# Optimization experiments

Measured on AMD Instinct MI355X. Metric: run time of the kernel, lower is better.

The kernel has to match this reference:

```python
import jax, jax.numpy as jnp
import numpy as np

B, R, L, D, V, P = 128, 30, 60, 300, 50000, 3

def setup_inputs() -> dict:
    key = jax.random.key(0)
    ks = jax.random.split(key, 24)
    u = lambda k, shp: jax.random.uniform(k, shp, jnp.float32, -0.1, 0.1)
    inp = {
        'user_reviews': jax.random.randint(ks[0], (B, R, L), 0, V),
        'item_reviews': jax.random.randint(ks[1], (B, R, L), 0, V),
        'user_emb': u(ks[2], (V, D)),
        'item_emb': u(ks[3], (V, D)),
        'g1_w': u(ks[4], (D, D)), 'g1_b': u(ks[5], (D,)),
        'g2_w': u(ks[6], (D, D)), 'g2_b': u(ks[7], (D,)),
        # per-pointer review-level co-attention params (gumbel=True, pooling=max)
        'Mr': jax.random.normal(ks[8], (P, D, D)),
        'Wur': jax.random.normal(ks[9], (P, D, D)) * 0.05, 'bur': jnp.zeros((P, D)),
        'Wir': jax.random.normal(ks[10], (P, D, D)) * 0.05, 'bir': jnp.zeros((P, D)),
        # per-pointer word-level co-attention params (gumbel=False, pooling=avg)
        'Mw': jax.random.normal(ks[11], (P, D, D)),
        'Wuw': jax.random.normal(ks[12], (P, D, D)) * 0.05, 'buw': jnp.zeros((P, D)),
        'Wiw': jax.random.normal(ks[13], (P, D, D)) * 0.05, 'biw': jnp.zeros((P, D)),
        # FM params, pred_in_dim = 2*P*D (pointer_agg='concat')
        'fm_w0': jnp.zeros((1,)),
        'fm_w': jnp.zeros((2 * P * D,)),
        'fm_v': jax.random.normal(ks[14], (2 * P * D, 10)) * 0.01,
    }
    return inp

def _review_gate(embs, g1_w, g1_b, g2_w, g2_b):
    # embs: [B,R,L,D] -> [B,R,D]
    s = embs.sum(2)
    return jax.nn.sigmoid(s @ g1_w.T + g1_b) * jnp.tanh(s @ g2_w.T + g2_b)

def _coatt_scores(u_fea, i_fea, Wu, bu, Wi, bi, M):
    u = u_fea @ Wu.T + bu
    i = i_fea @ Wi.T + bi
    return jnp.einsum('brd,de,bse->brs', u, M, i)  # [B,R,R] or [B,L,L]

def reference(user_reviews, item_reviews, user_emb, item_emb,
              g1_w, g1_b, g2_w, g2_b,
              Mr, Wur, bur, Wir, bir,
              Mw, Wuw, buw, Wiw, biw,
              fm_w0, fm_w, fm_v):
    gkey = jax.random.key(42)
    u_embs = user_emb[user_reviews]  # [B,R,L,D]
    i_embs = item_emb[item_reviews]
    u_rev = _review_gate(u_embs, g1_w, g1_b, g2_w, g2_b)  # [B,R,D]
    i_rev = _review_gate(i_embs, g1_w, g1_b, g2_w, g2_b)
    u_reps, i_reps = [], []
    for p in range(P):
        # review-level co-attention, max pooling, gumbel hard (top-1 pointer)
        s = _coatt_scores(u_rev, i_rev, Wur[p], bur[p], Wir[p], bir[p], Mr[p])
        u_score = s.max(2)   # [B,R]
        i_score = s.max(1)   # [B,R]
        gu = jax.random.gumbel(jax.random.fold_in(gkey, 2 * p), u_score.shape)
        gi = jax.random.gumbel(jax.random.fold_in(gkey, 2 * p + 1), i_score.shape)
        # hard one-hot bmm gather + .long() re-embed == argmax review select
        # (the .long() cast in torch severs the straight-through grad path)
        idx_u = jnp.argmax(u_score + gu, axis=1)  # [B]
        idx_i = jnp.argmax(i_score + gi, axis=1)
        u_tok = jnp.take_along_axis(user_reviews, idx_u[:, None, None], axis=1)[:, 0]  # [B,L]
        i_tok = jnp.take_along_axis(item_reviews, idx_i[:, None, None], axis=1)[:, 0]
        u_words = user_emb[u_tok]  # [B,L,D]
        i_words = item_emb[i_tok]
        # word-level co-attention, avg pooling, soft attention
        s2 = _coatt_scores(u_words, i_words, Wuw[p], buw[p], Wiw[p], biw[p], Mw[p])
        p_u = jax.nn.softmax(s2.mean(2), axis=1)  # [B,L]
        p_i = jax.nn.softmax(s2.mean(1), axis=1)
        u_reps.append(jnp.einsum('bld,bl->bd', u_words, p_u))
        i_reps.append(jnp.einsum('bld,bl->bd', i_words, p_i))
    u_fea = jnp.concatenate(u_reps, axis=1)  # [B, P*D] (pointer_agg='concat')
    i_fea = jnp.concatenate(i_reps, axis=1)
    joint = jnp.concatenate([u_fea, i_fea], axis=1)  # [B, 2*P*D]; dropout is identity (eval)
    # Factorization Machine
    linear = fm_w0 + jnp.sum(fm_w * joint, axis=1, keepdims=True)
    inter = 0.5 * jnp.sum((joint @ fm_v) ** 2 - (joint ** 2) @ (fm_v ** 2), axis=1, keepdims=True)
    return (linear + inter)[:, 0]  # [B]
```

## Files before the change

kernel.cpp:

```cpp
#include <hip/hip_runtime.h>
#include <stdint.h>
#include <math.h>


__host__ __device__ static inline void tf2x32(uint32_t k0, uint32_t k1,
                                              uint32_t x0, uint32_t x1,
                                              uint32_t* o0, uint32_t* o1) {
  uint32_t ks[3] = {k0, k1, k0 ^ k1 ^ 0x1BD11BDAu};
  x0 += ks[0]; x1 += ks[1];
  const int rotA[4] = {13, 15, 26, 6};
  const int rotB[4] = {17, 29, 16, 24};
#pragma unroll
  for (int i = 0; i < 5; ++i) {
    const int* rot = ((i & 1) == 0) ? rotA : rotB;
#pragma unroll
    for (int j = 0; j < 4; ++j) {
      x0 += x1;
      x1 = (x1 << rot[j]) | (x1 >> (32 - rot[j]));
      x1 ^= x0;
    }
    x0 += ks[(i + 1) % 3];
    x1 += ks[(i + 2) % 3] + (uint32_t)(i + 1);
  }
  *o0 = x0; *o1 = x1;
}

struct GKeys { uint32_t v[12]; };
struct Ptr6 {
  const float* X[6];
  const float* W[6];
  const float* Bb[6];
  float*       Y[6];
};

__device__ static inline float jax_gumbel32(uint32_t k0, uint32_t k1, uint32_t idx) {
  uint32_t o0, o1;
  tf2x32(k0, k1, 0u, idx, &o0, &o1);
  uint32_t bits = o0 ^ o1;
  float f = __uint_as_float((bits >> 9) | 0x3f800000u) - 1.0f;
  float u = (f > 0.0f) ? f : 1.17549435e-38f;
  return -logf(-logf(u));
}

#define MODE_NN 0
#define MODE_NT 1
#define MODE_TN 2

template <int MODE, bool BIAS>
__device__ __forceinline__ void gemm_tile(float* __restrict__ sm,
                                          const float* __restrict__ X,
                                          const float* __restrict__ W,
                                          const float* __restrict__ bias,
                                          float* __restrict__ Y,
                                          float* __restrict__ Yt,
                                          int M, int bm, int n0, int t) {
  float (*Xs)[68] = (float(*)[68])sm;
  float (*Ws_)[68] = (float(*)[68])(sm + 20 * 68);
  const bool act = t < 256;
  int tm4 = ((t >> 4) & 15) * 4;
  int tn4 = (t & 15) * 4;
  float acc[4][4] = {{0.f}};
  int xm = t >> 2;
  int xk = (t & 3) * 5;
  for (int k0 = 0; k0 < 300; k0 += 20) {
    if (act) {
      if (MODE == MODE_TN) {
#pragma unroll
        for (int i = 0; i < 5; ++i) {
          int flat = t + i * 256;
          int kk = flat >> 6, nn = flat & 63;
          int r = bm + nn;
          Xs[kk][nn] = (r < 300) ? X[(size_t)(k0 + kk) * 300 + r] : 0.f;
        }
      } else {
        int rr = bm + xm; if (rr >= M) rr = M - 1;
        const float* xp = X + (size_t)rr * 300 + k0 + xk;
#pragma unroll
        for (int j = 0; j < 5; ++j) Xs[xk + j][xm] = xp[j];
      }
      if (MODE == MODE_NT) {
        int d = n0 + xm;
        bool ok = d < 300;
        const float* wp = W + (size_t)d * 300 + k0 + xk;
#pragma unroll
        for (int j = 0; j < 5; ++j) Ws_[xk + j][xm] = ok ? wp[j] : 0.f;
      } else {
#pragma unroll
        for (int i = 0; i < 5; ++i) {
          int flat = t + i * 256;
          int kk = flat >> 6, nn = flat & 63;
          int col = n0 + nn;
          Ws_[kk][nn] = (col < 300) ? W[(size_t)(k0 + kk) * 300 + col] : 0.f;
        }
      }
    }
    __syncthreads();
    if (act) {
#pragma unroll
      for (int kk = 0; kk < 20; ++kk) {
        const float4 a = *(const float4*)&Xs[kk][tm4];
        const float4 w = *(const float4*)&Ws_[kk][tn4];
        float av[4] = {a.x, a.y, a.z, a.w};
        float wv[4] = {w.x, w.y, w.z, w.w};
#pragma unroll
        for (int i = 0; i < 4; ++i)
#pragma unroll
          for (int j = 0; j < 4; ++j)
            acc[i][j] = fmaf(av[i], wv[j], acc[i][j]);
      }
    }
    __syncthreads();
  }
  if (!act) return;
  float bv[4] = {0.f, 0.f, 0.f, 0.f};
  if (BIAS) {
#pragma unroll
    for (int j = 0; j < 4; ++j) {
      int col = n0 + tn4 + j;
      if (col < 300) bv[j] = bias[col];
    }
  }
#pragma unroll
  for (int i = 0; i < 4; ++i) {
    int row = bm + tm4 + i;
    if (row < M) {
      float* yp = Y + (size_t)row * 300 + n0 + tn4;
#pragma unroll
      for (int j = 0; j < 4; ++j) {
        int col = n0 + tn4 + j;
        if (col < 300) yp[j] = acc[i][j] + bv[j];
      }
    }
  }
  if (Yt) {
#pragma unroll
    for (int i = 0; i < 4; ++i) {
      int row = bm + tm4 + i;
      if (row < 300) {
#pragma unroll
        for (int j = 0; j < 4; ++j) {
          int col = n0 + tn4 + j;
          if (col < 300) Yt[(size_t)col * 300 + row] = acc[i][j];
        }
      }
    }
  }
}

__global__ __launch_bounds__(320)
void gather_kernel(const int* __restrict__ uRevs, const int* __restrict__ iRevs,
                   const float* __restrict__ uEmb, const float* __restrict__ iEmb,
                   float* __restrict__ S) {
  int bid = blockIdx.x;
  int t = threadIdx.x;
  __shared__ int toks[4][60];
  if (t < 240) {
    int rr = t / 60, l = t - rr * 60;
    int grow = bid * 4 + rr;
    int side = grow / 3840;
    int row = grow - side * 3840;
    const int* revs = side ? iRevs : uRevs;
    toks[rr][l] = revs[row * 60 + l];
  }
  __syncthreads();
  if (t < 300) {
    int sub = t / 75;
    int q4 = (t - sub * 75) * 4;
    int grow = bid * 4 + sub;
    int side = grow / 3840;
    const float* emb = side ? iEmb : uEmb;
    const int* tk = toks[sub];
    float ax = 0.f, ay = 0.f, az = 0.f, aw = 0.f;
#pragma unroll
    for (int l0 = 0; l0 < 60; l0 += 15) {
      float4 v[15];
#pragma unroll
      for (int qq = 0; qq < 15; ++qq)
        v[qq] = *(const float4*)&emb[(size_t)tk[l0 + qq] * 300 + q4];
#pragma unroll
      for (int qq = 0; qq < 15; ++qq) {
        ax += v[qq].x; ay += v[qq].y; az += v[qq].z; aw += v[qq].w;
      }
    }
    float4 r = {ax, ay, az, aw};
    *(float4*)&S[(size_t)grow * 300 + q4] = r;
  }
}

__global__ __launch_bounds__(256)
void gate_kernel(const float* __restrict__ S,
                 const float* __restrict__ g1w, const float* __restrict__ g1b,
                 const float* __restrict__ g2w, const float* __restrict__ g2b,
                 float* __restrict__ REV,
                 const float* __restrict__ Wur, const float* __restrict__ Mr,
                 const float* __restrict__ Mw, const float* __restrict__ Wiw,
                 const float* __restrict__ Wuw,
                 const float* __restrict__ bur, const float* __restrict__ buw,
                 const float* __restrict__ biw,
                 float* __restrict__ Wp, float* __restrict__ A1,
                 float* __restrict__ CGH, float* __restrict__ Bp) {
  __shared__ __align__(16) float arena[4080];
  int bid = blockIdx.x, t = threadIdx.x;
  if (bid < 600) {
    float (*Xs)[68] = (float(*)[68])arena;
    float (*Ws1)[68] = (float(*)[68])(arena + 1360);
    float (*Ws2)[68] = (float(*)[68])(arena + 2720);
    int bm = (bid / 5) * 64;
    int n0 = (bid % 5) * 64;
    int tm4 = (t >> 4) * 4;
    int tn4 = (t & 15) * 4;
    float acc1[4][4] = {{0.f}};
    float acc2[4][4] = {{0.f}};
    int xm = t >> 2;
    int xk = (t & 3) * 5;
    for (int k0 = 0; k0 < 300; k0 += 20) {
      const float* xp = S + (size_t)(bm + xm) * 300 + k0 + xk;
#pragma unroll
      for (int j = 0; j < 5; ++j) Xs[xk + j][xm] = xp[j];
      {
        int dIdx = n0 + xm;
        bool ok = dIdx < 300;
        const float* wp1 = g1w + (size_t)dIdx * 300 + k0 + xk;
        const float* wp2 = g2w + (size_t)dIdx * 300 + k0 + xk;
#pragma unroll
        for (int j = 0; j < 5; ++j) Ws1[xk + j][xm] = ok ? wp1[j] : 0.f;
#pragma unroll
        for (int j = 0; j < 5; ++j) Ws2[xk + j][xm] = ok ? wp2[j] : 0.f;
      }
      __syncthreads();
#pragma unroll
      for (int kk = 0; kk < 20; ++kk) {
        const float4 a = *(const float4*)&Xs[kk][tm4];
        const float4 w1 = *(const float4*)&Ws1[kk][tn4];
        const float4 w2 = *(const float4*)&Ws2[kk][tn4];
        float av[4] = {a.x, a.y, a.z, a.w};
        float w1v[4] = {w1.x, w1.y, w1.z, w1.w};
        float w2v[4] = {w2.x, w2.y, w2.z, w2.w};
#pragma unroll
        for (int i = 0; i < 4; ++i)
#pragma unroll
          for (int j = 0; j < 4; ++j) {
            acc1[i][j] = fmaf(av[i], w1v[j], acc1[i][j]);
            acc2[i][j] = fmaf(av[i], w2v[j], acc2[i][j]);
          }
      }
      __syncthreads();
    }
#pragma unroll
    for (int i = 0; i < 4; ++i) {
      int row = bm + tm4 + i;
      float* yp = REV + (size_t)row * 300 + n0 + tn4;
#pragma unroll
      for (int j = 0; j < 4; ++j) {
        int col = n0 + tn4 + j;
        if (col < 300) {
          float a = acc1[i][j] + g1b[col];
          float b = acc2[i][j] + g2b[col];
          yp[j] = (1.f / (1.f + expf(-a))) * tanhf(b);
        }
      }
    }
  } else if (bid < 675) {
    int zi = bid - 600, z = zi / 25, r = zi % 25;
    gemm_tile<MODE_TN, false>(arena, Wur + (size_t)z * 90000, Mr + (size_t)z * 90000,
                              nullptr, Wp + (size_t)z * 90000, nullptr,
                              300, (r / 5) * 64, (r % 5) * 64, t);
  } else if (bid < 750) {
    int zi = bid - 675, z = zi / 25, r = zi % 25;
    gemm_tile<MODE_NN, false>(arena, Mw + (size_t)z * 90000, Wiw + (size_t)z * 90000,
                              nullptr, A1 + (size_t)z * 90000, nullptr,
                              300, (r / 5) * 64, (r % 5) * 64, t);
  } else {
    int z = bid - 750;
    float* vb = arena;
    float* t1s = arena + 304;
    float* t2s = arena + 608;
    const float* Mwz = Mw + (size_t)z * 90000;
    const float* Wuwz = Wuw + (size_t)z * 90000;
    const float* Wiwz = Wiw + (size_t)z * 90000;
    const float* Mrz = Mr + (size_t)z * 90000;
    for (int k = t; k < 300; k += 256) vb[k] = biw[z * 300 + k];
    __syncthreads();
    {
      int w = t >> 6, j = t & 63;
      for (int i = 0; i < 75; ++i) {
        int e = w * 75 + i;
        float partial = 0.f;
#pragma unroll
        for (int c = 0; c < 5; ++c) {
          int k = j + c * 64;
          if (k < 300) partial = fmaf(Mwz[(size_t)e * 300 + k], vb[k], partial);
        }
#pragma unroll
        for (int m = 32; m >= 1; m >>= 1) partial += __shfl_xor(partial, m);
        if (j == 0) t1s[e] = partial;
      }
    }
    __syncthreads();
    for (int k = t; k < 300; k += 256) {
      float a = 0.f;
      for (int d = 0; d < 300; ++d) a = fmaf(Wuwz[(size_t)d * 300 + k], t1s[d], a);
      CGH[(size_t)(2 * z) * 300 + k] = a;
    }
    __syncthreads();
    for (int d = t; d < 300; d += 256) vb[d] = buw[z * 300 + d];
    __syncthreads();
    for (int e = t; e < 300; e += 256) {
      float a = 0.f;
      for (int d = 0; d < 300; ++d) a = fmaf(Mwz[(size_t)d * 300 + e], vb[d], a);
      t2s[e] = a;
    }
    __syncthreads();
    for (int k = t; k < 300; k += 256) {
      float a = 0.f;
      for (int e = 0; e < 300; ++e) a = fmaf(Wiwz[(size_t)e * 300 + k], t2s[e], a);
      CGH[(size_t)(2 * z + 1) * 300 + k] = a;
    }
    __syncthreads();
    for (int d = t; d < 300; d += 256) vb[d] = bur[z * 300 + d];
    __syncthreads();
    for (int e = t; e < 300; e += 256) {
      float a = 0.f;
      for (int d = 0; d < 300; ++d) a = fmaf(Mrz[(size_t)d * 300 + e], vb[d], a);
      Bp[z * 300 + e] = a;
    }
  }
}

__global__ __launch_bounds__(256)
void rev128_kernel(Ptr6 P, const float* __restrict__ Wuw,
                   const float* __restrict__ A1,
                   float* __restrict__ KG, float* __restrict__ KGT) {
  __shared__ __align__(16) float arena[4080];
  int bid = blockIdx.x, t = threadIdx.x;
  if (bid >= 900) {
    int zi = bid - 900, z = zi / 25, r = zi % 25;
    gemm_tile<MODE_TN, false>(arena, Wuw + (size_t)z * 90000, A1 + (size_t)z * 90000,
                              nullptr, KG + (size_t)z * 90000,
                              KGT + (size_t)z * 90000,
                              300, (r / 5) * 64, (r % 5) * 64, t);
    return;
  }
  int z = bid / 150;
  int rem = bid - z * 150;
  int bm = (rem % 30) * 128;
  int n0 = (rem / 30) * 64;
  const bool nt = z >= 3;
  const float* __restrict__ X = P.X[z];
  const float* __restrict__ W = P.W[z];
  const float* __restrict__ bias = P.Bb[z];
  float* __restrict__ Y = P.Y[z];
  float (*Xs)[136] = (float(*)[136])arena;
  float (*Ws_)[68] = (float(*)[68])(arena + 2720);
  int tm8 = (t >> 4) * 8, tn4 = (t & 15) * 4;
  float acc[8][4] = {{0.f}};
  int xm = t >> 1, xk = (t & 1) * 10;
  int wm = t >> 2, wk = (t & 3) * 5;
  for (int k0 = 0; k0 < 300; k0 += 20) {
    const float* xp = X + (size_t)(bm + xm) * 300 + k0 + xk;
#pragma unroll
    for (int j = 0; j < 10; ++j) Xs[xk + j][xm] = xp[j];
    if (nt) {
      int d = n0 + wm;
      bool ok = d < 300;
      const float* wp = W + (size_t)d * 300 + k0 + wk;
#pragma unroll
      for (int j = 0; j < 5; ++j) Ws_[wk + j][wm] = ok ? wp[j] : 0.f;
    } else {
#pragma unroll
      for (int i = 0; i < 5; ++i) {
        int flat = t + i * 256;
        int kk = flat >> 6, nn = flat & 63;
        int col = n0 + nn;
        Ws_[kk][nn] = (col < 300) ? W[(size_t)(k0 + kk) * 300 + col] : 0.f;
      }
    }
    __syncthreads();
#pragma unroll
    for (int kk = 0; kk < 20; ++kk) {
      const float4 a0 = *(const float4*)&Xs[kk][tm8];
      const float4 a1 = *(const float4*)&Xs[kk][tm8 + 4];
      const float4 w = *(const float4*)&Ws_[kk][tn4];
      float av[8] = {a0.x, a0.y, a0.z, a0.w, a1.x, a1.y, a1.z, a1.w};
      float wv[4] = {w.x, w.y, w.z, w.w};
#pragma unroll
      for (int i = 0; i < 8; ++i)
#pragma unroll
        for (int j = 0; j < 4; ++j)
          acc[i][j] = fmaf(av[i], wv[j], acc[i][j]);
    }
    __syncthreads();
  }
  float bv[4];
#pragma unroll
  for (int j = 0; j < 4; ++j) {
    int col = n0 + tn4 + j;
    bv[j] = (col < 300) ? bias[col] : 0.f;
  }
#pragma unroll
  for (int i = 0; i < 8; ++i) {
    float* yp = Y + (size_t)(bm + tm8 + i) * 300 + n0 + tn4;
#pragma unroll
    for (int j = 0; j < 4; ++j) {
      int col = n0 + tn4 + j;
      if (col < 300) yp[j] = acc[i][j] + bv[j];
    }
  }
}

__global__ __launch_bounds__(256)
void argmax_mean_kernel(const float* __restrict__ Tall, const float* __restrict__ Iall,
                        const int* __restrict__ uRevs, const int* __restrict__ iRevs,
                        const float* __restrict__ uEmb, const float* __restrict__ iEmb,
                        int* __restrict__ idxU, int* __restrict__ idxI,
                        float* __restrict__ MEAN, GKeys K) {
  int b = blockIdx.x, z = blockIdx.y, t = threadIdx.x;
  uint32_t ku0 = K.v[z * 4], ku1 = K.v[z * 4 + 1];
  uint32_t ki0 = K.v[z * 4 + 2], ki1 = K.v[z * 4 + 3];
  __shared__ __align__(16) float Is[30 * 304];
  __shared__ float Sc[900];
  __shared__ float us[30], vs[30];
  __shared__ int selU, selI;
  __shared__ int toksI_s[60], toksU_s[60];
  const float* Tb = Tall + (size_t)z * 1152000 + (size_t)b * 9000;
  const float* Ib = Iall + (size_t)z * 1152000 + (size_t)b * 9000;
  for (int fc = t; fc < 2250; fc += 256) {
    int r = fc / 75, q = fc - r * 75;
    *(float4*)&Is[r * 304 + q * 4] = *(const float4*)&Ib[r * 300 + q * 4];
  }
  __syncthreads();
  for (int id = t; id < 900; id += 256) {
    int r = id / 30, c = id - r * 30;
    const float* tr = Tb + r * 300;
    const float* ic = Is + c * 304;
    float acc = 0.f;
    for (int k = 0; k < 300; k += 4) {
      float4 a = *(const float4*)&tr[k];
      float4 w = *(const float4*)&ic[k];
      acc = fmaf(a.x, w.x, acc);
      acc = fmaf(a.y, w.y, acc);
      acc = fmaf(a.z, w.z, acc);
      acc = fmaf(a.w, w.w, acc);
    }
    Sc[id] = acc;
  }
  __syncthreads();
  if (t < 30) {
    float m = -3.4e38f;
    for (int c = 0; c < 30; ++c) m = fmaxf(m, Sc[t * 30 + c]);
    us[t] = m + jax_gumbel32(ku0, ku1, (uint32_t)(b * 30 + t));
  } else if (t >= 64 && t < 94) {
    int s = t - 64;
    float m = -3.4e38f;
    for (int r = 0; r < 30; ++r) m = fmaxf(m, Sc[r * 30 + s]);
    vs[s] = m + jax_gumbel32(ki0, ki1, (uint32_t)(b * 30 + s));
  }
  __syncthreads();
  if (t == 0) {
    int best = 0; float bvv = us[0];
    for (int r = 1; r < 30; ++r) { if (us[r] > bvv) { bvv = us[r]; best = r; } }
    idxU[z * 128 + b] = best; selU = best;
  } else if (t == 1) {
    int best = 0; float bvv = vs[0];
    for (int s = 1; s < 30; ++s) { if (vs[s] > bvv) { bvv = vs[s]; best = s; } }
    idxI[z * 128 + b] = best; selI = best;
  }
  __syncthreads();
  if (t < 60) toksI_s[t] = iRevs[(b * 30 + selI) * 60 + t];
  else if (t >= 64 && t < 124) toksU_s[t - 64] = uRevs[(b * 30 + selU) * 60 + (t - 64)];
  __syncthreads();
  for (int dd = t; dd < 600; dd += 256) {
    int side = dd / 300;
    int d = dd - side * 300;
    const int* tk = side ? toksU_s : toksI_s;
    const float* em = side ? uEmb : iEmb;
    float acc = 0.f;
#pragma unroll
    for (int l0 = 0; l0 < 60; l0 += 10) {
      float v[10];
#pragma unroll
      for (int q = 0; q < 10; ++q)
        v[q] = em[(size_t)tk[l0 + q] * 300 + d];
#pragma unroll
      for (int q = 0; q < 10; ++q) acc += v[q];
    }
    MEAN[((size_t)(2 * z + side) * 128 + b) * 300 + d] = acc * (1.f / 60.f);
  }
}

__global__ __launch_bounds__(256)
void word_rep_kernel(const int* __restrict__ uRevs, const int* __restrict__ iRevs,
                     const float* __restrict__ uEmb, const float* __restrict__ iEmb,
                     const int* __restrict__ idxU, const int* __restrict__ idxI,
                     const float* __restrict__ MEAN, const float* __restrict__ KG,
                     const float* __restrict__ KGT, const float* __restrict__ CGH,
                     float* __restrict__ JNT) {
  int b = blockIdx.x, side = blockIdx.y, p = blockIdx.z;
  int zz = 2 * p + side;
  const int* revs = side ? iRevs : uRevs;
  const float* emb = side ? iEmb : uEmb;
  int idx = side ? idxI[p * 128 + b] : idxU[p * 128 + b];
  const float* Kmat = (side ? KGT : KG) + (size_t)p * 90000;
  __shared__ int toks[60];
  __shared__ float ms[300];
  __shared__ float g_s[300];
  __shared__ float score[60];
  __shared__ float probs[64];
  int t = threadIdx.x;
  if (t < 60) toks[t] = revs[(b * 30 + idx) * 60 + t];
  const float* mrow = MEAN + ((size_t)zz * 128 + b) * 300;
  for (int d = t; d < 300; d += 256) ms[d] = mrow[d];
  __syncthreads();
  for (int k = t; k < 300; k += 256) {
    const float* kr = Kmat + (size_t)k * 300;
    float acc = 0.f;
    for (int e = 0; e < 300; e += 4) {
      float4 kv = *(const float4*)&kr[e];
      acc = fmaf(kv.x, ms[e], acc);
      acc = fmaf(kv.y, ms[e + 1], acc);
      acc = fmaf(kv.z, ms[e + 2], acc);
      acc = fmaf(kv.w, ms[e + 3], acc);
    }
    g_s[k] = acc + CGH[(size_t)zz * 300 + k];
  }
  __syncthreads();
  int w = t >> 6, j = t & 63;
  for (int i = 0; i < 15; ++i) {
    int l = w * 15 + i;
    const float* er = emb + (size_t)toks[l] * 300;
    float partial = 0.f;
#pragma unroll
    for (int c = 0; c < 5; ++c) {
      int k = j + c * 64;
      if (k < 300) partial = fmaf(er[k], g_s[k], partial);
    }
#pragma unroll
    for (int m = 32; m >= 1; m >>= 1) partial += __shfl_xor(partial, m);
    if (j == 0) score[l] = partial;
  }
  __syncthreads();
  if (w == 0) {
    float s = (j < 60) ? score[j] : -3.4e38f;
    float m = s;
#pragma unroll
    for (int mm = 32; mm >= 1; mm >>= 1) m = fmaxf(m, __shfl_xor(m, mm));
    float e = (j < 60) ? expf(s - m) : 0.f;
    float sum = e;
#pragma unroll
    for (int mm = 32; mm >= 1; mm >>= 1) sum += __shfl_xor(sum, mm);
    if (j < 60) probs[j] = e / sum;
  }
  __syncthreads();
  float* outp = JNT + (size_t)b * 1800 + side * 900 + p * 300;
  for (int d = t; d < 300; d += 256) {
    float acc = 0.f;
    for (int l0 = 0; l0 < 60; l0 += 6) {
      float e0 = emb[(size_t)toks[l0 + 0] * 300 + d];
      float e1 = emb[(size_t)toks[l0 + 1] * 300 + d];
      float e2 = emb[(size_t)toks[l0 + 2] * 300 + d];
      float e3 = emb[(size_t)toks[l0 + 3] * 300 + d];
      float e4 = emb[(size_t)toks[l0 + 4] * 300 + d];
      float e5 = emb[(size_t)toks[l0 + 5] * 300 + d];
      acc = fmaf(probs[l0 + 0], e0, acc);
      acc = fmaf(probs[l0 + 1], e1, acc);
      acc = fmaf(probs[l0 + 2], e2, acc);
      acc = fmaf(probs[l0 + 3], e3, acc);
      acc = fmaf(probs[l0 + 4], e4, acc);
      acc = fmaf(probs[l0 + 5], e5, acc);
    }
    outp[d] = acc;
  }
}

__global__ __launch_bounds__(64)
void fm_kernel(const float* __restrict__ JNT, const float* __restrict__ w0,
               const float* __restrict__ fw, const float* __restrict__ fv,
               float* __restrict__ out) {
  int b = blockIdx.x, lane = threadIdx.x;
  const float* x = JNT + (size_t)b * 1800;
  float lin = 0.f;
  float t1[10], t2[10];
#pragma unroll
  for (int k = 0; k < 10; ++k) { t1[k] = 0.f; t2[k] = 0.f; }
  for (int j = lane; j < 1800; j += 64) {
    float xv = x[j];
    lin = fmaf(fw[j], xv, lin);
    float xx = xv * xv;
#pragma unroll
    for (int k = 0; k < 10; ++k) {
      float v = fv[j * 10 + k];
      t1[k] = fmaf(xv, v, t1[k]);
      t2[k] = fmaf(xx, v * v, t2[k]);
    }
  }
#pragma unroll
  for (int m = 32; m >= 1; m >>= 1) {
    lin += __shfl_xor(lin, m);
#pragma unroll
    for (int k = 0; k < 10; ++k) {
      t1[k] += __shfl_xor(t1[k], m);
      t2[k] += __shfl_xor(t2[k], m);
    }
  }
  if (lane == 0) {
    float inter = 0.f;
#pragma unroll
    for (int k = 0; k < 10; ++k) inter += t1[k] * t1[k] - t2[k];
    out[b] = w0[0] + lin + 0.5f * inter;
  }
}

extern "C" void kernel_launch(void* const* d_in, const int* in_sizes, int n_in,
                              void* d_out, int out_size, void* d_ws, size_t ws_size,
                              hipStream_t stream) {
  (void)in_sizes; (void)n_in; (void)out_size;
  const int*   uRevs = (const int*)d_in[0];
  const int*   iRevs = (const int*)d_in[1];
  const float* uEmb  = (const float*)d_in[2];
  const float* iEmb  = (const float*)d_in[3];
  const float* g1w   = (const float*)d_in[4];
  const float* g1b   = (const float*)d_in[5];
  const float* g2w   = (const float*)d_in[6];
  const float* g2b   = (const float*)d_in[7];
  const float* Mr    = (const float*)d_in[8];
  const float* Wur   = (const float*)d_in[9];
  const float* bur   = (const float*)d_in[10];
  const float* Wir   = (const float*)d_in[11];
  const float* bir   = (const float*)d_in[12];
  const float* Mw    = (const float*)d_in[13];
  const float* Wuw   = (const float*)d_in[14];
  const float* buw   = (const float*)d_in[15];
  const float* Wiw   = (const float*)d_in[16];
  const float* biw   = (const float*)d_in[17];
  const float* fmw0  = (const float*)d_in[18];
  const float* fmw   = (const float*)d_in[19];
  const float* fmv   = (const float*)d_in[20];
  float* out = (float*)d_out;

  float* ws = (float*)d_ws;
  const size_t NEED_BYTES = (size_t)10298700 * 4;
  if (ws_size < NEED_BYTES) return;

  float* S     = ws + 0;
  float* TPall = ws + 0;
  float* REV   = ws + 3456000;
  float* MEAN  = ws + 3456000;
  float* JNT   = ws + 3916800;
  int*   idxU  = (int*)(ws + 4147200);
  int*   idxI  = idxU + 384;
  float* IPall = ws + 5760000;
  float* A1    = ws + 9216000;
  float* Wp    = ws + 9486000;
  float* KG    = ws + 9756000;
  float* KGT   = ws + 10026000;
  float* Bp    = ws + 10296000;
  float* CGH   = ws + 10296900;

  gather_kernel<<<dim3(1920), dim3(320), 0, stream>>>(
      uRevs, iRevs, uEmb, iEmb, S);

  gate_kernel<<<dim3(753), dim3(256), 0, stream>>>(
      S, g1w, g1b, g2w, g2b, REV,
      Wur, Mr, Mw, Wiw, Wuw, bur, buw, biw, Wp, A1, CGH, Bp);

  {
    Ptr6 P;
    for (int z = 0; z < 3; ++z) {
      P.X[z] = REV;
      P.W[z] = Wp + (size_t)z * 90000;
      P.Bb[z] = Bp + z * 300;
      P.Y[z] = TPall + (size_t)z * 1152000;
      P.X[z + 3] = REV + (size_t)3840 * 300;
      P.W[z + 3] = Wir + (size_t)z * 90000;
      P.Bb[z + 3] = bir + z * 300;
      P.Y[z + 3] = IPall + (size_t)z * 1152000;
    }
    rev128_kernel<<<dim3(975), dim3(256), 0, stream>>>(P, Wuw, A1, KG, KGT);
  }

  {
    GKeys K;
    for (int p = 0; p < 3; ++p) {
      tf2x32(0u, 42u, 0u, (uint32_t)(2 * p),     &K.v[p * 4],     &K.v[p * 4 + 1]);
      tf2x32(0u, 42u, 0u, (uint32_t)(2 * p + 1), &K.v[p * 4 + 2], &K.v[p * 4 + 3]);
    }
    argmax_mean_kernel<<<dim3(128, 3), dim3(256), 0, stream>>>(
        TPall, IPall, uRevs, iRevs, uEmb, iEmb, idxU, idxI, MEAN, K);
  }

  word_rep_kernel<<<dim3(128, 2, 3), dim3(256), 0, stream>>>(
      uRevs, iRevs, uEmb, iEmb, idxU, idxI, MEAN, KG, KGT, CGH, JNT);

  fm_kernel<<<dim3(128), dim3(64), 0, stream>>>(JNT, fmw0, fmw, fmv, out);
}
```

Baseline: 402.8 us.

## Split serial bias-vector chain blocks into parallel blocks across gate and rev kernels

Before, each pointer ran one block that computed a serial chain of five matrix-vector products, and these three blocks were likely the tail of gate_kernel. The chain is now split: the first-stage products (Mw·biw, Mw^T·buw, Mr^T·bur) are spread over several blocks in gate_kernel, and the second-stage products into CGH move into extra blocks of rev128_kernel. Intermediates now go through global workspace buffers T1S and T2S, and the inner loops load 15 rows at a time to get more memory-level parallelism. The cost is extra workspace and a dependency that now crosses the kernel boundary.

```diff
diff --git a/kernel.cpp b/kernel.cpp
--- a/kernel.cpp
+++ b/kernel.cpp
@@ -194,11 +194,11 @@
                  float* __restrict__ REV,
                  const float* __restrict__ Wur, const float* __restrict__ Mr,
                  const float* __restrict__ Mw, const float* __restrict__ Wiw,
-                 const float* __restrict__ Wuw,
                  const float* __restrict__ bur, const float* __restrict__ buw,
                  const float* __restrict__ biw,
                  float* __restrict__ Wp, float* __restrict__ A1,
-                 float* __restrict__ CGH, float* __restrict__ Bp) {
+                 float* __restrict__ T1S, float* __restrict__ T2S,
+                 float* __restrict__ Bp) {
   __shared__ __align__(16) float arena[4080];
   int bid = blockIdx.x, t = threadIdx.x;
   if (bid < 600) {
@@ -270,58 +270,61 @@
     gemm_tile<MODE_NN, false>(arena, Mw + (size_t)z * 90000, Wiw + (size_t)z * 90000,
                               nullptr, A1 + (size_t)z * 90000, nullptr,
                               300, (r / 5) * 64, (r % 5) * 64, t);
-  } else {
-    int z = bid - 750;
-    float* vb = arena;
-    float* t1s = arena + 304;
-    float* t2s = arena + 608;
+  } else if (bid < 762) {
+    int idx = bid - 750, z = idx >> 2, qb = idx & 3;
     const float* Mwz = Mw + (size_t)z * 90000;
-    const float* Wuwz = Wuw + (size_t)z * 90000;
-    const float* Wiwz = Wiw + (size_t)z * 90000;
-    const float* Mrz = Mr + (size_t)z * 90000;
-    for (int k = t; k < 300; k += 256) vb[k] = biw[z * 300 + k];
-    __syncthreads();
-    {
-      int w = t >> 6, j = t & 63;
-      for (int i = 0; i < 75; ++i) {
-        int e = w * 75 + i;
+    const float* bw = biw + z * 300;
+    int w = t >> 6, j = t & 63;
+    int e0 = qb * 75;
+    for (int i = 0; i < 19; ++i) {
+      int el = w + 4 * i;
+      if (el < 75) {
+        int e = e0 + el;
         float partial = 0.f;
 #pragma unroll
         for (int c = 0; c < 5; ++c) {
           int k = j + c * 64;
-          if (k < 300) partial = fmaf(Mwz[(size_t)e * 300 + k], vb[k], partial);
+          if (k < 300) partial = fmaf(Mwz[(size_t)e * 300 + k], bw[k], partial);
         }
 #pragma unroll
         for (int m = 32; m >= 1; m >>= 1) partial += __shfl_xor(partial, m);
-        if (j == 0) t1s[e] = partial;
-      }
-    }
-    __syncthreads();
-    for (int k = t; k < 300; k += 256) {
-      float a = 0.f;
-      for (int d = 0; d < 300; ++d) a = fmaf(Wuwz[(size_t)d * 300 + k], t1s[d], a);
-      CGH[(size_t)(2 * z) * 300 + k] = a;
-    }
-    __syncthreads();
+        if (j == 0) T1S[z * 300 + e] = partial;
+      }
+    }
+  } else if (bid < 768) {
+    int idx = bid - 762, z = idx >> 1, half = idx & 1;
+    const float* Mwz = Mw + (size_t)z * 90000;
+    float* vb = arena;
     for (int d = t; d < 300; d += 256) vb[d] = buw[z * 300 + d];
     __syncthreads();
-    for (int e = t; e < 300; e += 256) {
+    if (t < 150) {
+      int e = half * 150 + t;
       float a = 0.f;
-      for (int d = 0; d < 300; ++d) a = fmaf(Mwz[(size_t)d * 300 + e], vb[d], a);
-      t2s[e] = a;
-    }
-    __syncthreads();
-    for (int k = t; k < 300; k += 256) {
-      float a = 0.f;
-      for (int e = 0; e < 300; ++e) a = fmaf(Wiwz[(size_t)e * 300 + k], t2s[e], a);
-      CGH[(size_t)(2 * z + 1) * 300 + k] = a;
-    }
-    __syncthreads();
+      for (int d0 = 0; d0 < 300; d0 += 15) {
+        float mv[15];
+#pragma unroll
+        for (int q = 0; q < 15; ++q) mv[q] = Mwz[(size_t)(d0 + q) * 300 + e];
+#pragma unroll
+        for (int q = 0; q < 15; ++q) a = fmaf(mv[q], vb[d0 + q], a);
+      }
+      T2S[z * 300 + e] = a;
+    }
+  } else {
+    int idx = bid - 768, z = idx >> 1, half = idx & 1;
+    const float* Mrz = Mr + (size_t)z * 90000;
+    float* vb = arena;
     for (int d = t; d < 300; d += 256) vb[d] = bur[z * 300 + d];
     __syncthreads();
-    for (int e = t; e < 300; e += 256) {
+    if (t < 150) {
+      int e = half * 150 + t;
       float a = 0.f;
-      for (int d = 0; d < 300; ++d) a = fmaf(Mrz[(size_t)d * 300 + e], vb[d], a);
+      for (int d0 = 0; d0 < 300; d0 += 15) {
+        float mv[15];
+#pragma unroll
+        for (int q = 0; q < 15; ++q) mv[q] = Mrz[(size_t)(d0 + q) * 300 + e];
+#pragma unroll
+        for (int q = 0; q < 15; ++q) a = fmaf(mv[q], vb[d0 + q], a);
+      }
       Bp[z * 300 + e] = a;
     }
   }
@@ -329,10 +332,37 @@
 
 __global__ __launch_bounds__(256)
 void rev128_kernel(Ptr6 P, const float* __restrict__ Wuw,
+                   const float* __restrict__ Wiw,
                    const float* __restrict__ A1,
-                   float* __restrict__ KG, float* __restrict__ KGT) {
+                   float* __restrict__ KG, float* __restrict__ KGT,
+                   const float* __restrict__ T1S, const float* __restrict__ T2S,
+                   float* __restrict__ CGH) {
   __shared__ __align__(16) float arena[4080];
   int bid = blockIdx.x, t = threadIdx.x;
+  if (bid >= 975) {
+    int idx = bid - 975;
+    int z = idx >> 2;
+    int r2 = idx & 3;
+    int which = r2 >> 1, half = r2 & 1;
+    const float* W = (which ? Wiw : Wuw) + (size_t)z * 90000;
+    const float* tv = (which ? T2S : T1S) + z * 300;
+    float* vb = arena;
+    for (int d = t; d < 300; d += 256) vb[d] = tv[d];
+    __syncthreads();
+    if (t < 150) {
+      int k = half * 150 + t;
+      float a = 0.f;
+      for (int d0 = 0; d0 < 300; d0 += 15) {
+        float mv[15];
+#pragma unroll
+        for (int q = 0; q < 15; ++q) mv[q] = W[(size_t)(d0 + q) * 300 + k];
+#pragma unroll
+        for (int q = 0; q < 15; ++q) a = fmaf(mv[q], vb[d0 + q], a);
+      }
+      CGH[(size_t)(2 * z + which) * 300 + k] = a;
+    }
+    return;
+  }
   if (bid >= 900) {
     int zi = bid - 900, z = zi / 25, r = zi % 25;
     gemm_tile<MODE_TN, false>(arena, Wuw + (size_t)z * 90000, A1 + (size_t)z * 90000,
@@ -638,7 +668,7 @@
   float* out = (float*)d_out;
 
   float* ws = (float*)d_ws;
-  const size_t NEED_BYTES = (size_t)10298700 * 4;
+  const size_t NEED_BYTES = (size_t)10300500 * 4;
   if (ws_size < NEED_BYTES) return;
 
   float* S     = ws + 0;
@@ -655,13 +685,15 @@
   float* KGT   = ws + 10026000;
   float* Bp    = ws + 10296000;
   float* CGH   = ws + 10296900;
+  float* T1S   = ws + 10298700;
+  float* T2S   = ws + 10299600;
 
   gather_kernel<<<dim3(1920), dim3(320), 0, stream>>>(
       uRevs, iRevs, uEmb, iEmb, S);
 
-  gate_kernel<<<dim3(753), dim3(256), 0, stream>>>(
+  gate_kernel<<<dim3(774), dim3(256), 0, stream>>>(
       S, g1w, g1b, g2w, g2b, REV,
-      Wur, Mr, Mw, Wiw, Wuw, bur, buw, biw, Wp, A1, CGH, Bp);
+      Wur, Mr, Mw, Wiw, bur, buw, biw, Wp, A1, T1S, T2S, Bp);
 
   {
     Ptr6 P;
@@ -675,7 +707,8 @@
       P.Bb[z + 3] = bir + z * 300;
       P.Y[z + 3] = IPall + (size_t)z * 1152000;
     }
-    rev128_kernel<<<dim3(975), dim3(256), 0, stream>>>(P, Wuw, A1, KG, KGT);
+    rev128_kernel<<<dim3(987), dim3(256), 0, stream>>>(
+        P, Wuw, Wiw, A1, KG, KGT, T1S, T2S, CGH);
   }
 
   {
```

New measurement: 345.7 us. 1.17x faster.
